# Kernel optimization log

Measured on AMD Instinct MI355X. Metric: run time of the kernel, lower is better.

Reference implementation:

```python
import jax, jax.numpy as jnp
import numpy as np

L = 4        # num_layers
D = 1024     # transformer_dim
H = 16       # num_heads
HD = D // H  # head_dim
M = 4096     # mlp_dim
S = 1024     # seq_len
B = 2        # batch
WIN = 2      # temporal_window (one-sided)
EPS = 1e-5   # LayerNorm eps (torch default)


def setup_inputs() -> dict:
    key = jax.random.key(0)
    ks = jax.random.split(key, 16)
    def rn(k, shape, s=0.02):
        return jax.random.normal(k, shape, dtype=jnp.float32) * s
    return {
        "x": jax.random.normal(ks[0], (B, S, D), dtype=jnp.float32),
        # intra-frame MHA params (stacked over layers)
        "w_in1": rn(ks[1], (L, 3 * D, D)), "b_in1": jnp.zeros((L, 3 * D), jnp.float32),
        "w_out1": rn(ks[2], (L, D, D)),    "b_out1": jnp.zeros((L, D), jnp.float32),
        "ln1_g": jnp.ones((L, D), jnp.float32), "ln1_b": jnp.zeros((L, D), jnp.float32),
        # inter-frame (banded) MHA params
        "w_in2": rn(ks[3], (L, 3 * D, D)), "b_in2": jnp.zeros((L, 3 * D), jnp.float32),
        "w_out2": rn(ks[4], (L, D, D)),    "b_out2": jnp.zeros((L, D), jnp.float32),
        "ln2_g": jnp.ones((L, D), jnp.float32), "ln2_b": jnp.zeros((L, D), jnp.float32),
        # FFN params
        "ffn_w1": rn(ks[5], (L, M, D)), "ffn_b1": jnp.zeros((L, M), jnp.float32),
        "ffn_w2": rn(ks[6], (L, D, M)), "ffn_b2": jnp.zeros((L, D), jnp.float32),
        # final norm
        "lnf_g": jnp.ones((D,), jnp.float32), "lnf_b": jnp.zeros((D,), jnp.float32),
    }


def _layernorm(x, g, b):
    mu = jnp.mean(x, axis=-1, keepdims=True)
    var = jnp.mean(jnp.square(x - mu), axis=-1, keepdims=True)
    return (x - mu) * jax.lax.rsqrt(var + EPS) * g + b


def _mha(x, w_in, b_in, w_out, b_out, band):
    # x: [B,S,D]; w_in: [3D,D] packed qkv (torch in_proj layout)
    Bx, Sx, Dx = x.shape
    qkv = x @ w_in.T + b_in                      # [B,S,3D]
    q, k, v = jnp.split(qkv, 3, axis=-1)
    def to_heads(t):
        return t.reshape(Bx, Sx, H, HD).transpose(0, 2, 1, 3)  # [B,H,S,hd]
    q, k, v = to_heads(q), to_heads(k), to_heads(v)
    scores = jnp.einsum('bhsd,bhtd->bhst', q, k) / jnp.sqrt(jnp.float32(HD))
    if band is not None:
        scores = jnp.where(band, scores, -jnp.inf)  # additive -inf band mask
    attn = jax.nn.softmax(scores, axis=-1)
    out = jnp.einsum('bhst,bhtd->bhsd', attn, v)
    out = out.transpose(0, 2, 1, 3).reshape(Bx, Sx, Dx)
    return out @ w_out.T + b_out


def reference(x, w_in1, b_in1, w_out1, b_out1, ln1_g, ln1_b,
              w_in2, b_in2, w_out2, b_out2, ln2_g, ln2_b,
              ffn_w1, ffn_b1, ffn_w2, ffn_b2, lnf_g, lnf_b):
    idx = jnp.arange(S)
    band = jnp.abs(idx[:, None] - idx[None, :]) <= WIN  # [S,S] bool, True=attend
    for l in range(L):
        # intra-frame full MHA + residual + LN
        x_intra = _mha(x, w_in1[l], b_in1[l], w_out1[l], b_out1[l], None)
        x = _layernorm(x + x_intra, ln1_g[l], ln1_b[l])
        # inter-frame banded MHA + residual + LN
        x_inter = _mha(x, w_in2[l], b_in2[l], w_out2[l], b_out2[l], band)
        attended = _layernorm(x + x_inter, ln2_g[l], ln2_b[l])
        # FFN applied to attended; residual from attended (dropout_p=0)
        h = jax.nn.gelu(attended @ ffn_w1[l].T + ffn_b1[l], approximate=False)
        x = attended + (h @ ffn_w2[l].T + ffn_b2[l])
    return _layernorm(x, lnf_g, lnf_b)
```

## Files before the change

kernel.cpp:

```cpp
#include <hip/hip_runtime.h>
#include <math.h>

#define SEQ    1024
#define DIM    1024
#define NH     16
#define HDIM   64
#define MLP    4096
#define NLAYER 4
#define BATCH  2
#define NTOK   (BATCH * SEQ)
#define LN_EPS 1e-5f

typedef unsigned short ushortx;
typedef __attribute__((ext_vector_type(8))) short bf16x8;
typedef __attribute__((ext_vector_type(8))) unsigned short u16x8;
typedef __attribute__((ext_vector_type(4))) float f32x4;

__device__ __forceinline__ float gelu_exact(float x) {
    return 0.5f * x * (1.0f + erff(x * 0.70710678118654752f));
}
__device__ __forceinline__ unsigned int pack2bf(float a, float b) {
    union { float f; unsigned int u; } va, vb;
    va.f = a; vb.f = b;
    unsigned int ua = va.u + 0x7fffu + ((va.u >> 16) & 1u);
    unsigned int ub = vb.u + 0x7fffu + ((vb.u >> 16) & 1u);
    return (ua >> 16) | (ub & 0xffff0000u);
}
__device__ __forceinline__ ushortx bf16lo(float a) {
    return (ushortx)(pack2bf(a, 0.f) & 0xffffu);
}
__device__ __forceinline__ float bf2f(ushortx u) {
    union { unsigned int i; float f; } v; v.i = ((unsigned int)u) << 16; return v.f;
}

__global__ __launch_bounds__(256)
void cvt_w(const float* __restrict__ s0, const float* __restrict__ s1,
           const float* __restrict__ s2, const float* __restrict__ s3,
           const float* __restrict__ s4, const float* __restrict__ s5,
           ushortx* __restrict__ dst)
{
    const size_t total = 4194304;
    for (size_t g = (size_t)blockIdx.x * 256 + threadIdx.x; g < total;
         g += (size_t)gridDim.x * 256) {
        const float* src; size_t base;
        if      (g <  786432) { src = s0; base = 0; }
        else if (g < 1048576) { src = s1; base =  786432; }
        else if (g < 1835008) { src = s2; base = 1048576; }
        else if (g < 2097152) { src = s3; base = 1835008; }
        else if (g < 3145728) { src = s4; base = 2097152; }
        else                  { src = s5; base = 3145728; }
        float4 f = *(const float4*)(src + (g - base) * 4);
        ushort4 o = { bf16lo(f.x), bf16lo(f.y), bf16lo(f.z), bf16lo(f.w) };
        *(ushort4*)(dst + g * 4) = o;
    }
}

__global__ __launch_bounds__(256)
void init_x(const float* __restrict__ x0, float* __restrict__ xb,
            ushortx* __restrict__ xbf)
{
    const size_t i = (size_t)blockIdx.x * 256 + threadIdx.x;
    const float v = x0[i];
    xb[i] = v;
    xbf[i] = bf16lo(v);
}

template<int BM, int BN, int MODE>
__global__ __launch_bounds__(256)
void gemm_bf(const ushortx* __restrict__ A, const ushortx* __restrict__ W,
             const float* __restrict__ bias, void* __restrict__ Cout,
             void* __restrict__ Vout, int K, int N)
{
    constexpr int MT = BM / 32, NT = BN / 32;
    constexpr int AI = BM / 32, WI = BN / 32;
    __shared__ ushortx As[BM][72];
    __shared__ ushortx Ws[BN][72];
    const int t = threadIdx.x;
    const int wave = t >> 6, lane = t & 63, quad = lane >> 4, l16 = lane & 15;
    const int wm = (wave >> 1) * (BM / 2);
    const int wn = (wave & 1) * (BN / 2);
    const int rowBase = blockIdx.y * BM, colBase = blockIdx.x * BN;

    f32x4 acc[MT][NT];
    #pragma unroll
    for (int mt = 0; mt < MT; ++mt)
        #pragma unroll
        for (int nt = 0; nt < NT; ++nt) acc[mt][nt] = (f32x4){0.f, 0.f, 0.f, 0.f};

    u16x8 aR[AI], wR[WI];
    #pragma unroll
    for (int i = 0; i < AI; ++i) {
        const int c = t + 256 * i, r = c >> 3, c8 = (c & 7) * 8;
        aR[i] = *(const u16x8*)(A + (size_t)(rowBase + r) * K + c8);
    }
    #pragma unroll
    for (int i = 0; i < WI; ++i) {
        const int c = t + 256 * i, r = c >> 3, c8 = (c & 7) * 8;
        wR[i] = *(const u16x8*)(W + (size_t)(colBase + r) * K + c8);
    }
    const int nIt = K / 64;
    for (int kt = 0; kt < nIt; ++kt) {
        __syncthreads();
        #pragma unroll
        for (int i = 0; i < AI; ++i) {
            const int c = t + 256 * i;
            *(u16x8*)&As[c >> 3][(c & 7) * 8] = aR[i];
        }
        #pragma unroll
        for (int i = 0; i < WI; ++i) {
            const int c = t + 256 * i;
            *(u16x8*)&Ws[c >> 3][(c & 7) * 8] = wR[i];
        }
        __syncthreads();
        if (kt + 1 < nIt) {
            const int k0 = (kt + 1) * 64;
            #pragma unroll
            for (int i = 0; i < AI; ++i) {
                const int c = t + 256 * i, r = c >> 3, c8 = (c & 7) * 8;
                aR[i] = *(const u16x8*)(A + (size_t)(rowBase + r) * K + k0 + c8);
            }
            #pragma unroll
            for (int i = 0; i < WI; ++i) {
                const int c = t + 256 * i, r = c >> 3, c8 = (c & 7) * 8;
                wR[i] = *(const u16x8*)(W + (size_t)(colBase + r) * K + k0 + c8);
            }
        }
        #pragma unroll
        for (int kk = 0; kk < 2; ++kk) {
            bf16x8 af[MT], bfv[NT];
            #pragma unroll
            for (int mt = 0; mt < MT; ++mt)
                af[mt] = *(const bf16x8*)&As[wm + mt * 16 + l16][kk * 32 + quad * 8];
            #pragma unroll
            for (int nt = 0; nt < NT; ++nt)
                bfv[nt] = *(const bf16x8*)&Ws[wn + nt * 16 + l16][kk * 32 + quad * 8];
            #pragma unroll
            for (int mt = 0; mt < MT; ++mt)
                #pragma unroll
                for (int nt = 0; nt < NT; ++nt)
                    acc[mt][nt] = __builtin_amdgcn_mfma_f32_16x16x32_bf16(
                        af[mt], bfv[nt], acc[mt][nt], 0, 0, 0);
        }
    }
    #pragma unroll
    for (int mt = 0; mt < MT; ++mt) {
        #pragma unroll
        for (int nt = 0; nt < NT; ++nt) {
            const int colTile = colBase + wn + nt * 16;
            const int col = colTile + l16;
            const float bv = bias[col];
            const int rbase = rowBase + wm + mt * 16 + quad * 4;
            if (MODE == 0) {
                float* C = (float*)Cout;
                #pragma unroll
                for (int r = 0; r < 4; ++r)
                    C[(size_t)(rbase + r) * N + col] = acc[mt][nt][r] + bv;
            } else if (MODE == 1) {
                ushortx* C = (ushortx*)Cout;
                #pragma unroll
                for (int r = 0; r < 4; ++r)
                    C[(size_t)(rbase + r) * N + col] = bf16lo(gelu_exact(acc[mt][nt][r] + bv));
            } else if (MODE == 3) {
                ushortx* C = (ushortx*)Cout;
                #pragma unroll
                for (int r = 0; r < 4; ++r)
                    C[(size_t)(rbase + r) * (3 * DIM) + col] = bf16lo(acc[mt][nt][r] + bv);
            } else {
                if (colTile < 2 * DIM) {
                    ushortx* C = (ushortx*)Cout;
                    #pragma unroll
                    for (int r = 0; r < 4; ++r)
                        C[(size_t)(rbase + r) * (2 * DIM) + col] = bf16lo(acc[mt][nt][r] + bv);
                } else {
                    ushortx* vt = (ushortx*)Vout;
                    const int cb = col - 2 * DIM;
                    const int hh = cb >> 6, dd = cb & 63;
                    const int bb = rbase >> 10, s0 = rbase & 1023;
                    ushort4 pk = { bf16lo(acc[mt][nt][0] + bv), bf16lo(acc[mt][nt][1] + bv),
                                   bf16lo(acc[mt][nt][2] + bv), bf16lo(acc[mt][nt][3] + bv) };
                    *(ushort4*)&vt[((size_t)((bb * 16 + hh) * 64 + dd) << 10) + s0] = pk;
                }
            }
        }
    }
}

__global__ __launch_bounds__(256)
void attn_full(const ushortx* __restrict__ qk, const ushortx* __restrict__ vt,
               ushortx* __restrict__ outb)
{
    __shared__ ushortx Qs[64][72];
    __shared__ ushortx Ks[2][64][72];
    __shared__ ushortx VT[2][64][72];
    __shared__ ushortx Ps[4][16][72];

    const int blk = blockIdx.x;
    const int q0 = (blk & 15) * 64;
    const int h  = (blk >> 4) & 15;
    const int b  = blk >> 8;
    const int t  = threadIdx.x;
    const int w = t >> 6, lane = t & 63;
    const int quad = lane >> 4, l16 = lane & 15;

    const int c0 = t,       r0 = c0 >> 3, c80 = (c0 & 7) * 8;
    const int c1 = t + 256, r1 = c1 >> 3, c81 = (c1 & 7) * 8;

    *(u16x8*)&Qs[r0][c80] =
        *(const u16x8*)(qk + (size_t)(b * SEQ + q0 + r0) * (2 * DIM) + h * HDIM + c80);
    *(u16x8*)&Qs[r1][c81] =
        *(const u16x8*)(qk + (size_t)(b * SEQ + q0 + r1) * (2 * DIM) + h * HDIM + c81);

    const ushortx* kbase = qk + (size_t)(b * SEQ) * (2 * DIM) + DIM + h * HDIM;
    const ushortx* vbase = vt + ((size_t)((b * 16 + h) * 64) << 10);

    u16x8 kR0 = *(const u16x8*)(kbase + (size_t)r0 * (2 * DIM) + c80);
    u16x8 kR1 = *(const u16x8*)(kbase + (size_t)r1 * (2 * DIM) + c81);
    u16x8 vR0 = *(const u16x8*)(vbase + ((size_t)r0 << 10) + c80);
    u16x8 vR1 = *(const u16x8*)(vbase + ((size_t)r1 << 10) + c81);

    __syncthreads();
    bf16x8 aq0 = *(const bf16x8*)&Qs[w * 16 + l16][quad * 8];
    bf16x8 aq1 = *(const bf16x8*)&Qs[w * 16 + l16][32 + quad * 8];

    float m_r[4] = {-1e30f, -1e30f, -1e30f, -1e30f};
    float l_r[4] = {0.f, 0.f, 0.f, 0.f};
    f32x4 Oa[4];
    #pragma unroll
    for (int nt = 0; nt < 4; ++nt) Oa[nt] = (f32x4){0.f, 0.f, 0.f, 0.f};

    int buf = 0;
    for (int kt = 0; kt < SEQ / 64; ++kt) {
        *(u16x8*)&Ks[buf][r0][c80] = kR0;
        *(u16x8*)&Ks[buf][r1][c81] = kR1;
        *(u16x8*)&VT[buf][r0][c80] = vR0;
        *(u16x8*)&VT[buf][r1][c81] = vR1;
        __syncthreads();

        if (kt + 1 < SEQ / 64) {
            const int k0 = (kt + 1) * 64;
            kR0 = *(const u16x8*)(kbase + (size_t)(k0 + r0) * (2 * DIM) + c80);
            kR1 = *(const u16x8*)(kbase + (size_t)(k0 + r1) * (2 * DIM) + c81);
            vR0 = *(const u16x8*)(vbase + ((size_t)r0 << 10) + k0 + c80);
            vR1 = *(const u16x8*)(vbase + ((size_t)r1 << 10) + k0 + c81);
        }

        f32x4 s[4];
        #pragma unroll
        for (int nt = 0; nt < 4; ++nt) {
            bf16x8 bk0 = *(const bf16x8*)&Ks[buf][nt * 16 + l16][quad * 8];
            bf16x8 bk1 = *(const bf16x8*)&Ks[buf][nt * 16 + l16][32 + quad * 8];
            s[nt] = __builtin_amdgcn_mfma_f32_16x16x32_bf16(aq0, bk0,
                        (f32x4){0.f, 0.f, 0.f, 0.f}, 0, 0, 0);
            s[nt] = __builtin_amdgcn_mfma_f32_16x16x32_bf16(aq1, bk1, s[nt], 0, 0, 0);
        }
        float tm[4], alpha[4];
        #pragma unroll
        for (int r = 0; r < 4; ++r) {
            float v = fmaxf(fmaxf(s[0][r], s[1][r]), fmaxf(s[2][r], s[3][r])) * 0.125f;
            #pragma unroll
            for (int off = 1; off < 16; off <<= 1) v = fmaxf(v, __shfl_xor(v, off));
            tm[r] = v;
        }
        #pragma unroll
        for (int r = 0; r < 4; ++r) {
            const float mn = fmaxf(m_r[r], tm[r]);
            alpha[r] = __expf(m_r[r] - mn);
            m_r[r] = mn;
        }
        float rs[4] = {0.f, 0.f, 0.f, 0.f};
        #pragma unroll
        for (int nt = 0; nt < 4; ++nt) {
            #pragma unroll
            for (int r = 0; r < 4; ++r) {
                const float p = __expf(s[nt][r] * 0.125f - m_r[r]);
                rs[r] += p;
                Ps[w][quad * 4 + r][nt * 16 + l16] = bf16lo(p);
            }
        }
        #pragma unroll
        for (int r = 0; r < 4; ++r) {
            float v = rs[r];
            #pragma unroll
            for (int off = 1; off < 16; off <<= 1) v += __shfl_xor(v, off);
            l_r[r] = l_r[r] * alpha[r] + v;
            #pragma unroll
            for (int nt = 0; nt < 4; ++nt) Oa[nt][r] *= alpha[r];
        }
        bf16x8 pa0 = *(const bf16x8*)&Ps[w][l16][quad * 8];
        bf16x8 pa1 = *(const bf16x8*)&Ps[w][l16][32 + quad * 8];
        #pragma unroll
        for (int nt = 0; nt < 4; ++nt) {
            bf16x8 bv0 = *(const bf16x8*)&VT[buf][nt * 16 + l16][quad * 8];
            bf16x8 bv1 = *(const bf16x8*)&VT[buf][nt * 16 + l16][32 + quad * 8];
            Oa[nt] = __builtin_amdgcn_mfma_f32_16x16x32_bf16(pa0, bv0, Oa[nt], 0, 0, 0);
            Oa[nt] = __builtin_amdgcn_mfma_f32_16x16x32_bf16(pa1, bv1, Oa[nt], 0, 0, 0);
        }
        buf ^= 1;
    }
    float inv[4];
    #pragma unroll
    for (int r = 0; r < 4; ++r) inv[r] = 1.f / l_r[r];
    #pragma unroll
    for (int r = 0; r < 4; ++r) {
        const size_t row = (size_t)(b * SEQ + q0 + w * 16 + quad * 4 + r);
        #pragma unroll
        for (int nt = 0; nt < 4; ++nt)
            outb[row * DIM + h * HDIM + nt * 16 + l16] = bf16lo(Oa[nt][r] * inv[r]);
    }
}

__global__ __launch_bounds__(256)
void attn_band(const ushortx* __restrict__ qkv, ushortx* __restrict__ outb)
{
    const int blk = blockIdx.x;
    const int chunk = blk & (SEQ / 32 - 1);
    const int h = (blk >> 5) & (NH - 1);
    const int b = blk >> 9;
    const int tid = threadIdx.x;
    const int s = chunk * 32 + (tid >> 3);
    const int oct = tid & 7;
    const size_t base = (size_t)(b * SEQ) * (3 * DIM) + h * HDIM + oct * 8;

    float qf[8];
    {
        u16x8 qv = *(const u16x8*)(qkv + base + (size_t)s * (3 * DIM));
        #pragma unroll
        for (int j = 0; j < 8; ++j) qf[j] = bf2f((ushortx)qv[j]);
    }

    float sc[5];
    #pragma unroll
    for (int o = 0; o < 5; ++o) {
        const int tt = s - 2 + o;
        const bool valid = ((unsigned)tt < SEQ);
        float d = 0.f;
        if (valid) {
            u16x8 kv = *(const u16x8*)(qkv + base + (size_t)tt * (3 * DIM) + DIM);
            #pragma unroll
            for (int j = 0; j < 8; ++j) d += qf[j] * bf2f((ushortx)kv[j]);
        }
        d += __shfl_xor(d, 1);
        d += __shfl_xor(d, 2);
        d += __shfl_xor(d, 4);
        sc[o] = valid ? d * 0.125f : -1e30f;
    }
    const float m = fmaxf(fmaxf(fmaxf(sc[0], sc[1]), fmaxf(sc[2], sc[3])), sc[4]);
    float p[5], sum = 0.f;
    #pragma unroll
    for (int o = 0; o < 5; ++o) { p[o] = __expf(sc[o] - m); sum += p[o]; }
    const float inv = 1.f / sum;

    float acc[8] = {0.f, 0.f, 0.f, 0.f, 0.f, 0.f, 0.f, 0.f};
    #pragma unroll
    for (int o = 0; o < 5; ++o) {
        const int tt = s - 2 + o;
        if ((unsigned)tt < SEQ) {
            u16x8 vv = *(const u16x8*)(qkv + base + (size_t)tt * (3 * DIM) + 2 * DIM);
            #pragma unroll
            for (int j = 0; j < 8; ++j) acc[j] += p[o] * bf2f((ushortx)vv[j]);
        }
    }
    unsigned int o01 = pack2bf(acc[0] * inv, acc[1] * inv);
    unsigned int o23 = pack2bf(acc[2] * inv, acc[3] * inv);
    unsigned int o45 = pack2bf(acc[4] * inv, acc[5] * inv);
    unsigned int o67 = pack2bf(acc[6] * inv, acc[7] * inv);
    uint4 st = { o01, o23, o45, o67 };
    *(uint4*)(outb + (size_t)(b * SEQ + s) * DIM + h * HDIM + oct * 8) = st;
}

__global__ __launch_bounds__(256)
void add_ln(const float* __restrict__ x, const float* __restrict__ y,
            const float* __restrict__ g, const float* __restrict__ be,
            float* __restrict__ outf, ushortx* __restrict__ outb, int hasY)
{
    __shared__ float row[DIM];
    __shared__ float red[256];
    const int n = blockIdx.x;
    const int tid = threadIdx.x;
    float lsum = 0.f;
    for (int i = tid; i < DIM; i += 256) {
        float v = x[(size_t)n * DIM + i];
        if (hasY) v += y[(size_t)n * DIM + i];
        row[i] = v;
        lsum += v;
    }
    red[tid] = lsum;
    __syncthreads();
    for (int ofs = 128; ofs > 0; ofs >>= 1) {
        if (tid < ofs) red[tid] += red[tid + ofs];
        __syncthreads();
    }
    const float mu = red[0] * (1.f / DIM);
    __syncthreads();
    float lvar = 0.f;
    for (int i = tid; i < DIM; i += 256) {
        const float d = row[i] - mu;
        lvar += d * d;
    }
    red[tid] = lvar;
    __syncthreads();
    for (int ofs = 128; ofs > 0; ofs >>= 1) {
        if (tid < ofs) red[tid] += red[tid + ofs];
        __syncthreads();
    }
    const float rstd = rsqrtf(red[0] * (1.f / DIM) + LN_EPS);
    __syncthreads();
    for (int i = tid; i < DIM; i += 256) {
        const float o = (row[i] - mu) * rstd * g[i] + be[i];
        if (outf) outf[(size_t)n * DIM + i] = o;
        if (outb) outb[(size_t)n * DIM + i] = bf16lo(o);
    }
}

__global__ __launch_bounds__(256)
void add_vec(const float* __restrict__ a, const float* __restrict__ b,
             float* __restrict__ outf, ushortx* __restrict__ outb)
{
    const size_t i = (size_t)blockIdx.x * 256 + threadIdx.x;
    const float v = a[i] + b[i];
    outf[i] = v;
    outb[i] = bf16lo(v);
}

extern "C" void kernel_launch(void* const* d_in, const int* in_sizes, int n_in,
                              void* d_out, int out_size, void* d_ws, size_t ws_size,
                              hipStream_t stream)
{
    const float* x0     = (const float*)d_in[0];
    const float* w_in1  = (const float*)d_in[1];
    const float* b_in1  = (const float*)d_in[2];
    const float* w_out1 = (const float*)d_in[3];
    const float* b_out1 = (const float*)d_in[4];
    const float* ln1_g  = (const float*)d_in[5];
    const float* ln1_b  = (const float*)d_in[6];
    const float* w_in2  = (const float*)d_in[7];
    const float* b_in2  = (const float*)d_in[8];
    const float* w_out2 = (const float*)d_in[9];
    const float* b_out2 = (const float*)d_in[10];
    const float* ln2_g  = (const float*)d_in[11];
    const float* ln2_b  = (const float*)d_in[12];
    const float* fw1    = (const float*)d_in[13];
    const float* fb1    = (const float*)d_in[14];
    const float* fw2    = (const float*)d_in[15];
    const float* fb2    = (const float*)d_in[16];
    const float* lnf_g  = (const float*)d_in[17];
    const float* lnf_b  = (const float*)d_in[18];
    float* out = (float*)d_out;

    char* W = (char*)d_ws;
    float*   xb    = (float*)(W);
    float*   t2    = (float*)(W + ((size_t)8  << 20));
    float*   attf  = (float*)(W + ((size_t)16 << 20));
    ushortx* actbf = (ushortx*)(W + ((size_t)24 << 20));
    ushortx* qkb   = (ushortx*)(W + ((size_t)28 << 20));
    ushortx* vtb   = (ushortx*)(W + ((size_t)36 << 20));
    ushortx* hbf   = (ushortx*)(W + ((size_t)28 << 20));
    ushortx* wbf   = (ushortx*)(W + ((size_t)44 << 20));

    const size_t OFF_WI1 = 0,        OFF_WO1 = 3145728;
    const size_t OFF_WI2 = 4194304,  OFF_WO2 = 7340032;
    const size_t OFF_W1  = 8388608,  OFF_W2  = 12582912;

    init_x<<<dim3(NTOK * DIM / 256), dim3(256), 0, stream>>>(x0, xb, actbf);

    const dim3 blk(256);
    for (int l = 0; l < NLAYER; ++l) {
        const float* bi1 = b_in1  + (size_t)l * 3 * DIM;
        const float* bo1 = b_out1 + (size_t)l * DIM;
        const float* g1  = ln1_g  + (size_t)l * DIM;
        const float* be1 = ln1_b  + (size_t)l * DIM;
        const float* bi2 = b_in2  + (size_t)l * 3 * DIM;
        const float* bo2 = b_out2 + (size_t)l * DIM;
        const float* g2  = ln2_g  + (size_t)l * DIM;
        const float* be2 = ln2_b  + (size_t)l * DIM;
        const float* b1l = fb1    + (size_t)l * MLP;
        const float* b2l = fb2    + (size_t)l * DIM;

        cvt_w<<<dim3(2048), blk, 0, stream>>>(
            w_in1 + (size_t)l * 3 * DIM * DIM, w_out1 + (size_t)l * DIM * DIM,
            w_in2 + (size_t)l * 3 * DIM * DIM, w_out2 + (size_t)l * DIM * DIM,
            fw1 + (size_t)l * MLP * DIM, fw2 + (size_t)l * DIM * MLP, wbf);

        gemm_bf<128, 128, 2><<<dim3(3 * DIM / 128, NTOK / 128), blk, 0, stream>>>(
            actbf, wbf + OFF_WI1, bi1, qkb, vtb, DIM, 0);
        attn_full<<<dim3(BATCH * NH * (SEQ / 64)), blk, 0, stream>>>(qkb, vtb, actbf);
        gemm_bf<64, 64, 0><<<dim3(DIM / 64, NTOK / 64), blk, 0, stream>>>(
            actbf, wbf + OFF_WO1, bo1, t2, nullptr, DIM, DIM);
        add_ln<<<dim3(NTOK), blk, 0, stream>>>(xb, t2, g1, be1, xb, actbf, 1);
        gemm_bf<128, 128, 3><<<dim3(3 * DIM / 128, NTOK / 128), blk, 0, stream>>>(
            actbf, wbf + OFF_WI2, bi2, qkb, nullptr, DIM, 3 * DIM);
        attn_band<<<dim3(BATCH * NH * (SEQ / 32)), blk, 0, stream>>>(qkb, actbf);
        gemm_bf<64, 64, 0><<<dim3(DIM / 64, NTOK / 64), blk, 0, stream>>>(
            actbf, wbf + OFF_WO2, bo2, t2, nullptr, DIM, DIM);
        add_ln<<<dim3(NTOK), blk, 0, stream>>>(xb, t2, g2, be2, attf, actbf, 1);
        gemm_bf<128, 128, 1><<<dim3(MLP / 128, NTOK / 128), blk, 0, stream>>>(
            actbf, wbf + OFF_W1, b1l, hbf, nullptr, DIM, MLP);
        gemm_bf<64, 64, 0><<<dim3(DIM / 64, NTOK / 64), blk, 0, stream>>>(
            hbf, wbf + OFF_W2, b2l, t2, nullptr, MLP, DIM);
        add_vec<<<dim3(NTOK * DIM / 256), blk, 0, stream>>>(attf, t2, xb, actbf);
    }
    add_ln<<<dim3(NTOK), blk, 0, stream>>>(xb, nullptr, lnf_g, lnf_b, out, nullptr, 0);
}
```

Baseline: 1.120 ms.

## Split-K the FFN down-projection GEMM with larger tiles and a four-way reduction

The FFN second GEMM moves from 64x64 tiles over the full K=4096 to 128x128 tiles split four ways along K on the grid z dimension. Slice 0 writes to t2 with the bias added, and slices 1-3 write fp32 partials into scratch space that reuses the already-consumed bf16 weight buffer. A new add_vec4 kernel sums the partials with the residual. Larger tiles are meant to improve data reuse while keeping the block count the same. The cost is extra fp32 partial-sum traffic to write and read back.

```diff
diff --git a/kernel.cpp b/kernel.cpp
--- a/kernel.cpp
+++ b/kernel.cpp
@@ -69,7 +69,7 @@
 __global__ __launch_bounds__(256)
 void gemm_bf(const ushortx* __restrict__ A, const ushortx* __restrict__ W,
              const float* __restrict__ bias, void* __restrict__ Cout,
-             void* __restrict__ Vout, int K, int N)
+             void* __restrict__ Vout, int K, int N, int kChunk)
 {
     constexpr int MT = BM / 32, NT = BN / 32;
     constexpr int AI = BM / 32, WI = BN / 32;
@@ -80,6 +80,7 @@
     const int wm = (wave >> 1) * (BM / 2);
     const int wn = (wave & 1) * (BN / 2);
     const int rowBase = blockIdx.y * BM, colBase = blockIdx.x * BN;
+    const int kBase = blockIdx.z * kChunk;
 
     f32x4 acc[MT][NT];
     #pragma unroll
@@ -91,14 +92,14 @@
     #pragma unroll
     for (int i = 0; i < AI; ++i) {
         const int c = t + 256 * i, r = c >> 3, c8 = (c & 7) * 8;
-        aR[i] = *(const u16x8*)(A + (size_t)(rowBase + r) * K + c8);
+        aR[i] = *(const u16x8*)(A + (size_t)(rowBase + r) * K + kBase + c8);
     }
     #pragma unroll
     for (int i = 0; i < WI; ++i) {
         const int c = t + 256 * i, r = c >> 3, c8 = (c & 7) * 8;
-        wR[i] = *(const u16x8*)(W + (size_t)(colBase + r) * K + c8);
-    }
-    const int nIt = K / 64;
+        wR[i] = *(const u16x8*)(W + (size_t)(colBase + r) * K + kBase + c8);
+    }
+    const int nIt = kChunk / 64;
     for (int kt = 0; kt < nIt; ++kt) {
         __syncthreads();
         #pragma unroll
@@ -113,7 +114,7 @@
         }
         __syncthreads();
         if (kt + 1 < nIt) {
-            const int k0 = (kt + 1) * 64;
+            const int k0 = kBase + (kt + 1) * 64;
             #pragma unroll
             for (int i = 0; i < AI; ++i) {
                 const int c = t + 256 * i, r = c >> 3, c8 = (c & 7) * 8;
@@ -148,10 +149,13 @@
         for (int nt = 0; nt < NT; ++nt) {
             const int colTile = colBase + wn + nt * 16;
             const int col = colTile + l16;
-            const float bv = bias[col];
+            const float bv = (blockIdx.z == 0) ? bias[col] : 0.f;
             const int rbase = rowBase + wm + mt * 16 + quad * 4;
             if (MODE == 0) {
-                float* C = (float*)Cout;
+                float* C = (blockIdx.z == 0)
+                    ? (float*)Cout
+                    : (float*)Vout + (size_t)(blockIdx.z - 1) *
+                          ((size_t)gridDim.y * BM) * N;
                 #pragma unroll
                 for (int r = 0; r < 4; ++r)
                     C[(size_t)(rbase + r) * N + col] = acc[mt][nt][r] + bv;
@@ -422,6 +426,18 @@
     outb[i] = bf16lo(v);
 }
 
+__global__ __launch_bounds__(256)
+void add_vec4(const float* __restrict__ a, const float* __restrict__ p0,
+              const float* __restrict__ p1, const float* __restrict__ p2,
+              const float* __restrict__ p3,
+              float* __restrict__ outf, ushortx* __restrict__ outb)
+{
+    const size_t i = (size_t)blockIdx.x * 256 + threadIdx.x;
+    const float v = a[i] + ((p0[i] + p1[i]) + (p2[i] + p3[i]));
+    outf[i] = v;
+    outb[i] = bf16lo(v);
+}
+
 extern "C" void kernel_launch(void* const* d_in, const int* in_sizes, int n_in,
                               void* d_out, int out_size, void* d_ws, size_t ws_size,
                               hipStream_t stream)
@@ -456,6 +472,7 @@
     ushortx* vtb   = (ushortx*)(W + ((size_t)36 << 20));
     ushortx* hbf   = (ushortx*)(W + ((size_t)28 << 20));
     ushortx* wbf   = (ushortx*)(W + ((size_t)44 << 20));
+    float*   pk1   = (float*)(W + ((size_t)44 << 20));
 
     const size_t OFF_WI1 = 0,        OFF_WO1 = 3145728;
     const size_t OFF_WI2 = 4194304,  OFF_WO2 = 7340032;
@@ -482,22 +499,24 @@
             fw1 + (size_t)l * MLP * DIM, fw2 + (size_t)l * DIM * MLP, wbf);
 
         gemm_bf<128, 128, 2><<<dim3(3 * DIM / 128, NTOK / 128), blk, 0, stream>>>(
-            actbf, wbf + OFF_WI1, bi1, qkb, vtb, DIM, 0);
+            actbf, wbf + OFF_WI1, bi1, qkb, vtb, DIM, 0, DIM);
         attn_full<<<dim3(BATCH * NH * (SEQ / 64)), blk, 0, stream>>>(qkb, vtb, actbf);
         gemm_bf<64, 64, 0><<<dim3(DIM / 64, NTOK / 64), blk, 0, stream>>>(
-            actbf, wbf + OFF_WO1, bo1, t2, nullptr, DIM, DIM);
+            actbf, wbf + OFF_WO1, bo1, t2, nullptr, DIM, DIM, DIM);
         add_ln<<<dim3(NTOK), blk, 0, stream>>>(xb, t2, g1, be1, xb, actbf, 1);
         gemm_bf<128, 128, 3><<<dim3(3 * DIM / 128, NTOK / 128), blk, 0, stream>>>(
-            actbf, wbf + OFF_WI2, bi2, qkb, nullptr, DIM, 3 * DIM);
+            actbf, wbf + OFF_WI2, bi2, qkb, nullptr, DIM, 3 * DIM, DIM);
         attn_band<<<dim3(BATCH * NH * (SEQ / 32)), blk, 0, stream>>>(qkb, actbf);
         gemm_bf<64, 64, 0><<<dim3(DIM / 64, NTOK / 64), blk, 0, stream>>>(
-            actbf, wbf + OFF_WO2, bo2, t2, nullptr, DIM, DIM);
+            actbf, wbf + OFF_WO2, bo2, t2, nullptr, DIM, DIM, DIM);
         add_ln<<<dim3(NTOK), blk, 0, stream>>>(xb, t2, g2, be2, attf, actbf, 1);
         gemm_bf<128, 128, 1><<<dim3(MLP / 128, NTOK / 128), blk, 0, stream>>>(
-            actbf, wbf + OFF_W1, b1l, hbf, nullptr, DIM, MLP);
-        gemm_bf<64, 64, 0><<<dim3(DIM / 64, NTOK / 64), blk, 0, stream>>>(
-            hbf, wbf + OFF_W2, b2l, t2, nullptr, MLP, DIM);
-        add_vec<<<dim3(NTOK * DIM / 256), blk, 0, stream>>>(attf, t2, xb, actbf);
+            actbf, wbf + OFF_W1, b1l, hbf, nullptr, DIM, MLP, DIM);
+        gemm_bf<128, 128, 0><<<dim3(DIM / 128, NTOK / 128, 4), blk, 0, stream>>>(
+            hbf, wbf + OFF_W2, b2l, t2, pk1, MLP, DIM, MLP / 4);
+        add_vec4<<<dim3(NTOK * DIM / 256), blk, 0, stream>>>(
+            attf, t2, pk1, pk1 + (size_t)NTOK * DIM, pk1 + (size_t)2 * NTOK * DIM,
+            xb, actbf);
     }
     add_ln<<<dim3(NTOK), blk, 0, stream>>>(xb, nullptr, lnf_g, lnf_b, out, nullptr, 0);
 }
```

Result: no change. 1.128 ms (+0.7%).
